# Kernel optimization log

Measured on AMD Instinct MI355X. Metric: run time of the kernel, lower is better.

Reference implementation:

```python
import jax, jax.numpy as jnp
import numpy as np

COST_POS = 5.0
COST_CONF = 1.0
LAMBDA_POS = 5.0
LAMBDA_CONF = 2.0
LAMBDA_NOOBJ = 0.5


def _lsa(cost):
    """Rectangular linear sum assignment (Jonker-Volgenant shortest augmenting
    path), same semantics as scipy.optimize.linear_sum_assignment."""
    cost = np.asarray(cost, dtype=np.float64)
    transposed = cost.shape[1] < cost.shape[0]
    if transposed:
        cost = cost.T
    nr, nc = cost.shape  # nr <= nc
    u = np.zeros(nr)
    v = np.zeros(nc)
    col4row = np.full(nr, -1, dtype=np.int64)
    row4col = np.full(nc, -1, dtype=np.int64)
    for cur_row in range(nr):
        shortest = np.full(nc, np.inf)
        pathback = np.full(nc, -1, dtype=np.int64)
        SR = np.zeros(nr, dtype=bool)
        SC = np.zeros(nc, dtype=bool)
        remaining = np.ones(nc, dtype=bool)
        min_val = 0.0
        i = cur_row
        sink = -1
        while sink == -1:
            SR[i] = True
            rem = np.flatnonzero(remaining)
            new_cost = min_val + cost[i, rem] - u[i] - v[rem]
            better = new_cost < shortest[rem]
            idx = rem[better]
            shortest[idx] = new_cost[better]
            pathback[idx] = i
            j = rem[np.argmin(shortest[rem])]
            min_val = shortest[j]
            remaining[j] = False
            SC[j] = True
            if row4col[j] == -1:
                sink = j
            else:
                i = row4col[j]
        u[cur_row] += min_val
        rows = np.flatnonzero(SR)
        rows = rows[rows != cur_row]
        u[rows] += min_val - shortest[col4row[rows]]
        v[SC] -= min_val - shortest[SC]
        j = sink
        while True:
            i = pathback[j]
            row4col[j] = i
            col4row[i], j = j, col4row[i]
            if i == cur_row:
                break
    if transposed:
        rows = col4row
        cols = np.arange(nr)
        order = np.argsort(rows)
        return rows[order], cols[order]
    return np.arange(nr), col4row


def _match(pred_c, conf, gt_c):
    """Per-image Hungarian matching (host-side, @no_grad in the original).
    cost = COST_POS * L1(pred, gt) - COST_CONF * sigmoid(conf)."""
    B, N, _ = pred_c.shape
    M = gt_c.shape[1]
    pred_idx = np.empty((B, M), dtype=np.int64)
    gt_idx = np.empty((B, M), dtype=np.int64)
    for b in range(B):
        c_pos = np.abs(pred_c[b][:, None, :] - gt_c[b][None, :, :]).sum(-1)  # [N,M]
        c_conf = -1.0 / (1.0 + np.exp(-conf[b]))  # [N]
        cost = COST_POS * c_pos + COST_CONF * c_conf[:, None]
        r, c = _lsa(cost)
        pred_idx[b] = r
        gt_idx[b] = c
    return pred_idx, gt_idx


def setup_inputs() -> dict:
    key = jax.random.key(0)
    B, N, M, D = 32, 300, 50, 2
    k1, k2, k3, k4, k5 = jax.random.split(key, 5)
    return {
        "pred_centroids": jax.random.uniform(k1, (B, N, D), dtype=jnp.float32),
        "pred_logits": jax.random.normal(k2, (B, N, 1), dtype=jnp.float32),
        "pred_conf": jax.random.normal(k3, (B, N), dtype=jnp.float32),
        "gt_centroids": jax.random.uniform(k4, (B, M, D), dtype=jnp.float32),
        "gt_classes": jax.random.randint(k5, (B, M), 0, 1),
    }


def reference(pred_centroids, pred_logits, pred_conf, gt_centroids, gt_classes):
    B, N, D = pred_centroids.shape
    M = gt_centroids.shape[1]
    # Matching indices are constants (computed under no_grad, host-side).
    pred_idx, gt_idx = _match(np.asarray(pred_centroids, np.float64),
                              np.asarray(pred_conf, np.float64),
                              np.asarray(gt_centroids, np.float64))
    pred_idx = jnp.asarray(pred_idx)  # [B,M]
    gt_idx = jnp.asarray(gt_idx)      # [B,M]
    b = jnp.arange(B)[:, None]
    mp = pred_centroids[b, pred_idx]  # [B,M,D]
    mg = gt_centroids[b, gt_idx]      # [B,M,D]
    # per-image L1 mean, summed over images (all images have M matches)
    loss_pos = jnp.mean(jnp.abs(mp - mg), axis=(1, 2)).sum()
    m_logit = pred_conf[b, pred_idx]  # [B,M]
    # BCE-with-logits, target=1: softplus(-x); target=0: softplus(x)
    loss_obj = jnp.mean(jax.nn.softplus(-m_logit), axis=1).sum()
    unmatched = jnp.ones((B, N), dtype=bool).at[b, pred_idx].set(False)
    sp = jax.nn.softplus(pred_conf)
    loss_noobj = (jnp.where(unmatched, sp, 0.0).sum(axis=1) / (N - M)).sum()
    loss_pos = LAMBDA_POS * loss_pos / B
    loss_conf_obj = LAMBDA_CONF * loss_obj / B
    loss_conf_noobj = LAMBDA_NOOBJ * loss_noobj / B
    loss_total = loss_pos + loss_conf_obj + loss_conf_noobj
    n_matched = jnp.asarray(float(M), dtype=jnp.float32)  # total matched / B
    return loss_pos, loss_conf_obj, loss_conf_noobj, loss_total, n_matched
```

## Files before the change

### kernel.cpp

```cpp
#include <hip/hip_runtime.h>
#include <math.h>


#define BB 32
#define NN 300
#define MM 50
#define KPL 5

#define F5(OP) OP(0) OP(1) OP(2) OP(3) OP(4)

__device__ __forceinline__ float softplus_f(float x) {
    return fmaxf(x, 0.0f) + __logf(1.0f + __expf(-fabsf(x)));
}
__device__ __forceinline__ float readlane_f(float x, int l) {
    return __int_as_float(__builtin_amdgcn_readlane(__float_as_int(x), l));
}
__device__ __forceinline__ int readlane_i(int x, int l) {
    return __builtin_amdgcn_readlane(x, l);
}
__device__ __forceinline__ unsigned umaxu(unsigned a, unsigned b) { return a > b ? a : b; }

__device__ __forceinline__ unsigned minkey_f32(float d) {
    unsigned s = (unsigned)__float_as_int(d);
    unsigned us = (s & 0x80000000u) ? ~s : (s | 0x80000000u);
    return ~us;
}
__device__ __forceinline__ float keydec_up(unsigned key) {
    unsigned us = (~key) | 0x1FFu;
    return (us & 0x80000000u) ? __uint_as_float(us & 0x7FFFFFFFu)
                              : __uint_as_float(~us);
}

__device__ __forceinline__ unsigned rowshr_maxkey(unsigned x) {
#define DPP_STEP(CTRL) { \
    unsigned t_ = (unsigned)__builtin_amdgcn_update_dpp(0, (int)x, CTRL, 0xF, 0xF, false); \
    x = umaxu(x, t_); }
    DPP_STEP(0x111)
    DPP_STEP(0x112)
    DPP_STEP(0x114)
    DPP_STEP(0x118)
#undef DPP_STEP
    return x;
}

__device__ __forceinline__ int div5(int n) { return (n * 52429) >> 18; }

__global__ __launch_bounds__(64, 1) void lsa_loss_kernel(
    const float* __restrict__ pred_c,
    const float* __restrict__ conf,
    const float* __restrict__ gt_c,
    float* __restrict__ ws)
{
    const int b = blockIdx.x;
    const int lane = threadIdx.x;
    const bool owns = lane < (NN / KPL);
    const int base_j = KPL * lane;

    __shared__ float4 s_px4[NN/4 + 1], s_py4[NN/4 + 1], s_cm4[NN/4 + 1];
    __shared__ int claimed[NN];
    float* s_px = (float*)s_px4;
    float* s_py = (float*)s_py4;
    float* s_cm2 = (float*)s_cm4;

#define DECL(k) float px5##k, py5##k, cf##k, cm##k, sh##k; int pb##k;
    F5(DECL)
#undef DECL
    unsigned r4cpack = 0;
    int rem;
    float u = 0.0f, gx5 = 0.0f, gy5 = 0.0f, u_sub = 0.0f;
    int col4row = -1;

#define LOADK(k) { \
        int j = base_j + k; \
        float vpx = 0.0f, vpy = 0.0f, vcf = 0.0f; \
        if (owns) { \
            float2 pc = *(const float2*)&pred_c[(b*NN + j)*2]; \
            vpx = pc.x; vpy = pc.y; \
            vcf = conf[b*NN + j]; \
        } \
        px5##k = 5.0f*vpx; py5##k = 5.0f*vpy; cf##k = vcf; \
        cm##k = -(1.0f / (1.0f + __expf(-vcf)));   }
    F5(LOADK)
#undef LOADK
    if (lane < MM) {
        float2 gc = *(const float2*)&gt_c[(b*MM + lane)*2];
        gx5 = 5.0f*gc.x;
        gy5 = 5.0f*gc.y;
    }
#define STAGE(k) if (owns) { int j = base_j + k; \
        s_px[j] = px5##k; s_py[j] = py5##k; s_cm2[j] = cm##k + 2.0f; \
        claimed[j] = 63; }
    F5(STAGE)
#undef STAGE
    if (lane == 63) {
        const float4 big = {1e30f, 1e30f, 1e30f, 1e30f};
        s_px4[NN/4] = big; s_py4[NN/4] = big; s_cm4[NN/4] = big;
    }
#define IDXF(k) const unsigned idx##k = (unsigned)(511 - (base_j + k));
    F5(IDXF)
#undef IDXF
    __syncthreads();

    unsigned bestkey = 0u;
#pragma unroll 2
    for (int j0 = 0; j0 < NN; j0 += 8) {
        float4 vxa = s_px4[(j0 >> 2) + 0], vxb = s_px4[(j0 >> 2) + 1];
        float4 vya = s_py4[(j0 >> 2) + 0], vyb = s_py4[(j0 >> 2) + 1];
        float4 vca = s_cm4[(j0 >> 2) + 0], vcb = s_cm4[(j0 >> 2) + 1];
        float c0 = fabsf(vxa.x - gx5) + fabsf(vya.x - gy5) + vca.x;
        float c1 = fabsf(vxa.y - gx5) + fabsf(vya.y - gy5) + vca.y;
        float c2 = fabsf(vxa.z - gx5) + fabsf(vya.z - gy5) + vca.z;
        float c3 = fabsf(vxa.w - gx5) + fabsf(vya.w - gy5) + vca.w;
        float c4 = fabsf(vxb.x - gx5) + fabsf(vyb.x - gy5) + vcb.x;
        float c5 = fabsf(vxb.y - gx5) + fabsf(vyb.y - gy5) + vcb.y;
        float c6 = fabsf(vxb.z - gx5) + fabsf(vyb.z - gy5) + vcb.z;
        float c7 = fabsf(vxb.w - gx5) + fabsf(vyb.w - gy5) + vcb.w;
        unsigned q0 = (~__float_as_uint(c0) & 0xFFFFFE00u) | (unsigned)(511 - j0);
        unsigned q1 = (~__float_as_uint(c1) & 0xFFFFFE00u) | (unsigned)(510 - j0);
        unsigned q2 = (~__float_as_uint(c2) & 0xFFFFFE00u) | (unsigned)(509 - j0);
        unsigned q3 = (~__float_as_uint(c3) & 0xFFFFFE00u) | (unsigned)(508 - j0);
        unsigned q4 = (~__float_as_uint(c4) & 0xFFFFFE00u) | (unsigned)(507 - j0);
        unsigned q5 = (~__float_as_uint(c5) & 0xFFFFFE00u) | (unsigned)(506 - j0);
        unsigned q6 = (~__float_as_uint(c6) & 0xFFFFFE00u) | (unsigned)(505 - j0);
        unsigned q7 = (~__float_as_uint(c7) & 0xFFFFFE00u) | (unsigned)(504 - j0);
        unsigned qa = umaxu(umaxu(q0, q1), umaxu(q2, q3));
        unsigned qb = umaxu(umaxu(q4, q5), umaxu(q6, q7));
        bestkey = umaxu(bestkey, umaxu(qa, qb));
    }
    int wantj = 511 - (int)(bestkey & 511u);
    if (lane < MM) {
        u = fabsf(s_px[wantj] - gx5) + fabsf(s_py[wantj] - gy5)
            + (s_cm2[wantj] - 2.0f);
        atomicMin(&claimed[wantj], lane);
    }
    __syncthreads();
    if (lane < MM && claimed[wantj] == lane) col4row = wantj;
#define RCINIT(k) { int w = owns ? claimed[base_j + k] : 63; \
        r4cpack |= ((w < 63) ? (unsigned)(w + 1) : 0u) << (6*k); }
    F5(RCINIT)
#undef RCINIT

    unsigned long long freerows = __ballot(lane < MM && col4row < 0);
    while (freerows) {
        int cur_row = (int)__ffsll(freerows) - 1;
        freerows &= freerows - 1ull;

#define RINIT(k) sh##k = INFINITY; pb##k = 0;
        F5(RINIT)
#undef RINIT
        rem = owns ? 0x1F : 0;
        unsigned long long sr_mask = 0ull;
        float min_val = 0.0f;
        int i = cur_row;
        int sink = -1;

        for (int pops = 0; pops <= NN && sink < 0; ++pops) {
            sr_mask |= (1ull << i);
            float u_i   = readlane_f(u,   i);
            float gx5_i = readlane_f(gx5, i);
            float gy5_i = readlane_f(gy5, i);
            float mvu = min_val - u_i;
            int ip1 = i + 1;

#define RELAX(k) { \
                float dx5 = fabsf(px5##k - gx5_i); \
                float dy5 = fabsf(py5##k - gy5_i); \
                float nc = dx5 + dy5 + (cm##k + mvu); \
                bool imp = (((rem >> k) & 1) != 0) && (nc < sh##k); \
                sh##k = imp ? nc : sh##k; \
                pb##k = imp ? ip1 : pb##k; }
            F5(RELAX)
#undef RELAX

#define KEYK(k) unsigned key##k = ((rem >> k) & 1) \
                ? ((minkey_f32(sh##k) & 0xFFFFFE00u) | idx##k) : 0u;
            F5(KEYK)
#undef KEYK
            unsigned lkey = umaxu(umaxu(umaxu(key0, key1), umaxu(key2, key3)), key4);

            unsigned acc = rowshr_maxkey(lkey);
            unsigned k0 = (unsigned)readlane_i((int)acc, 15);
            unsigned k1 = (unsigned)readlane_i((int)acc, 31);
            unsigned k2 = (unsigned)readlane_i((int)acc, 47);
            unsigned k3 = (unsigned)readlane_i((int)acc, 63);
            unsigned gkey = umaxu(umaxu(k0, k1), umaxu(k2, k3));
            if (gkey == 0u) { sink = 0; break; }

            int bestj = 511 - (int)(gkey & 511u);
            int srcl = div5(bestj);
            int qj = bestj - KPL*srcl;
            min_val = keydec_up(gkey);

            unsigned rp = (unsigned)readlane_i((int)r4cpack, srcl);
            int r4 = (int)((rp >> (qj*6)) & 63u) - 1;

            rem = (lane == srcl) ? (rem & ~(1 << qj)) : rem;
            if (r4 < 0 || r4 >= MM) {
                sink = bestj;
            } else {
                i = r4;
                u_sub = (lane == r4) ? min_val : u_sub;
            }
        }

        if (lane < MM) {
            if (lane == cur_row) u += min_val;
            else if ((sr_mask >> lane) & 1ull) u += min_val - u_sub;
        }
#define VUPD(k) if (owns && !((rem >> k) & 1)) cm##k += min_val - sh##k;
        F5(VUPD)
#undef VUPD

        int j = sink < 0 ? 0 : sink;
        for (int step = 0; step <= MM; ++step) {
            int tj = div5(j), qj2 = j - KPL*tj;
            int pbl = qj2==0?pb0:qj2==1?pb1:qj2==2?pb2:qj2==3?pb3:pb4;
            int pi = readlane_i(pbl, tj) - 1;
            if (pi < 0 || pi >= MM) break;
            int q6 = qj2*6;
            unsigned nv = (r4cpack & ~(63u << q6)) | ((unsigned)(pi+1) << q6);
            r4cpack = (lane == tj) ? nv : r4cpack;
            int c_old = readlane_i(col4row, pi);
            col4row = (lane == pi) ? j : col4row;
            j = c_old;
            if (pi == cur_row) break;
            if (j < 0 || j >= NN) break;
        }
    }

    float lp = 0.0f, lo = 0.0f, ln = 0.0f;
    if (lane < MM) {
        int j = (col4row < 0 || col4row >= NN) ? 0 : col4row;
        lp = 0.2f * (fabsf(s_px[j] - gx5) + fabsf(s_py[j] - gy5));
        lo = softplus_f(-conf[b*NN + j]);
    }
#define NOOBJ(k) if (owns && ((r4cpack >> (6*k)) & 63u) == 0u) \
        ln += softplus_f(cf##k);
    F5(NOOBJ)
#undef NOOBJ
    for (int off = 32; off > 0; off >>= 1) {
        lp += __shfl_xor(lp, off, 64);
        lo += __shfl_xor(lo, off, 64);
        ln += __shfl_xor(ln, off, 64);
    }
    if (lane == 0) {
        ws[b*4 + 0] = lp;
        ws[b*4 + 1] = lo;
        ws[b*4 + 2] = ln;
    }
}

__global__ __launch_bounds__(64, 1) void reduce_out_kernel(
    const float* __restrict__ ws, float* __restrict__ out)
{
    const int lane = threadIdx.x;
    float lp = 0.0f, lo = 0.0f, ln = 0.0f;
    if (lane < BB) {
        lp = ws[lane*4 + 0];
        lo = ws[lane*4 + 1];
        ln = ws[lane*4 + 2];
    }
    for (int off = 16; off > 0; off >>= 1) {
        lp += __shfl_xor(lp, off, 64);
        lo += __shfl_xor(lo, off, 64);
        ln += __shfl_xor(ln, off, 64);
    }
    if (lane == 0) {
        double cp = 5.0 * ((double)lp / (double)(MM*2))  / (double)BB;
        double co = 2.0 * ((double)lo / (double)MM)      / (double)BB;
        double cn = 0.5 * ((double)ln / (double)(NN-MM)) / (double)BB;
        out[0] = (float)cp;
        out[1] = (float)co;
        out[2] = (float)cn;
        out[3] = (float)(cp + co + cn);
        out[4] = 50.0f;
    }
}

extern "C" void kernel_launch(void* const* d_in, const int* in_sizes, int n_in,
                              void* d_out, int out_size, void* d_ws, size_t ws_size,
                              hipStream_t stream) {
    const float* pred_c = (const float*)d_in[0];
    const float* conf   = (const float*)d_in[2];
    const float* gt_c   = (const float*)d_in[3];
    float* out = (float*)d_out;
    float* ws  = (float*)d_ws;

    lsa_loss_kernel<<<BB, 64, 0, stream>>>(pred_c, conf, gt_c, ws);
    reduce_out_kernel<<<1, 64, 0, stream>>>(ws, out);
}
```

Baseline: 92.95 us.

## Split greedy initial column scan across four wavefronts per block

Launches 256 threads per image so four wavefronts each scan an 80-column slice of the cost matrix for the initial row-minimum pass, then merges the partial best keys through shared memory before wave 0 continues the augmenting-path phase alone. The shared padding is extended so the last slice reads sentinel values. Confidence logits are also staged in shared memory, so the final objectness loss reads from LDS instead of global memory. This adds a block barrier and idle waves during the serial Hungarian phase. The speedup is limited to the init scan, which is a small part of the total.

```diff
diff --git a/kernel.cpp b/kernel.cpp
--- a/kernel.cpp
+++ b/kernel.cpp
@@ -6,6 +6,8 @@
 #define NN 300
 #define MM 50
 #define KPL 5
+#define NWV 4
+#define CPW 80
 
 #define F5(OP) OP(0) OP(1) OP(2) OP(3) OP(4)
 
@@ -45,19 +47,23 @@
 
 __device__ __forceinline__ int div5(int n) { return (n * 52429) >> 18; }
 
-__global__ __launch_bounds__(64, 1) void lsa_loss_kernel(
+__global__ __launch_bounds__(NWV*64, 1) void lsa_loss_kernel(
     const float* __restrict__ pred_c,
     const float* __restrict__ conf,
     const float* __restrict__ gt_c,
     float* __restrict__ ws)
 {
     const int b = blockIdx.x;
-    const int lane = threadIdx.x;
-    const bool owns = lane < (NN / KPL);
-    const int base_j = KPL * lane;
-
-    __shared__ float4 s_px4[NN/4 + 1], s_py4[NN/4 + 1], s_cm4[NN/4 + 1];
+    const int tid = threadIdx.x;
+    const int wid = tid >> 6;
+    const int lane = tid & 63;
+    const bool owns = tid < (NN / KPL);
+    const int base_j = KPL * tid;
+
+    __shared__ float4 s_px4[NN/4 + 5], s_py4[NN/4 + 5], s_cm4[NN/4 + 5];
     __shared__ int claimed[NN];
+    __shared__ float s_cf[NN];
+    __shared__ unsigned s_part[NWV * 64];
     float* s_px = (float*)s_px4;
     float* s_py = (float*)s_py4;
     float* s_cm2 = (float*)s_cm4;
@@ -89,12 +95,13 @@
     }
 #define STAGE(k) if (owns) { int j = base_j + k; \
         s_px[j] = px5##k; s_py[j] = py5##k; s_cm2[j] = cm##k + 2.0f; \
-        claimed[j] = 63; }
+        s_cf[j] = cf##k; claimed[j] = 63; }
     F5(STAGE)
 #undef STAGE
-    if (lane == 63) {
+    if (tid >= 59 && tid < 64) {
         const float4 big = {1e30f, 1e30f, 1e30f, 1e30f};
-        s_px4[NN/4] = big; s_py4[NN/4] = big; s_cm4[NN/4] = big;
+        int p = 75 + (tid - 59);
+        s_px4[p] = big; s_py4[p] = big; s_cm4[p] = big;
     }
 #define IDXF(k) const unsigned idx##k = (unsigned)(511 - (base_j + k));
     F5(IDXF)
@@ -102,8 +109,9 @@
     __syncthreads();
 
     unsigned bestkey = 0u;
-#pragma unroll 2
-    for (int j0 = 0; j0 < NN; j0 += 8) {
+#pragma unroll
+    for (int t = 0; t < CPW/8; ++t) {
+        int j0 = wid*CPW + t*8;
         float4 vxa = s_px4[(j0 >> 2) + 0], vxb = s_px4[(j0 >> 2) + 1];
         float4 vya = s_py4[(j0 >> 2) + 0], vyb = s_py4[(j0 >> 2) + 1];
         float4 vca = s_cm4[(j0 >> 2) + 0], vcb = s_cm4[(j0 >> 2) + 1];
@@ -127,14 +135,26 @@
         unsigned qb = umaxu(umaxu(q4, q5), umaxu(q6, q7));
         bestkey = umaxu(bestkey, umaxu(qa, qb));
     }
-    int wantj = 511 - (int)(bestkey & 511u);
-    if (lane < MM) {
-        u = fabsf(s_px[wantj] - gx5) + fabsf(s_py[wantj] - gy5)
-            + (s_cm2[wantj] - 2.0f);
-        atomicMin(&claimed[wantj], lane);
-    }
+    s_part[wid*64 + lane] = bestkey;
     __syncthreads();
-    if (lane < MM && claimed[wantj] == lane) col4row = wantj;
+
+    if (wid == 0) {
+        bestkey = umaxu(umaxu(s_part[lane], s_part[64 + lane]),
+                        umaxu(s_part[128 + lane], s_part[192 + lane]));
+        int wantj = 511 - (int)(bestkey & 511u);
+        if (lane < MM) {
+            u = fabsf(s_px[wantj] - gx5) + fabsf(s_py[wantj] - gy5)
+                + (s_cm2[wantj] - 2.0f);
+            atomicMin(&claimed[wantj], lane);
+        }
+        col4row = -1 - wantj;
+    }
+    __syncthreads();
+    if (wid != 0) return;
+    {
+        int wantj = -1 - col4row;
+        col4row = (lane < MM && claimed[wantj] == lane) ? wantj : -1;
+    }
 #define RCINIT(k) { int w = owns ? claimed[base_j + k] : 63; \
         r4cpack |= ((w < 63) ? (unsigned)(w + 1) : 0u) << (6*k); }
     F5(RCINIT)
@@ -232,7 +252,7 @@
     if (lane < MM) {
         int j = (col4row < 0 || col4row >= NN) ? 0 : col4row;
         lp = 0.2f * (fabsf(s_px[j] - gx5) + fabsf(s_py[j] - gy5));
-        lo = softplus_f(-conf[b*NN + j]);
+        lo = softplus_f(-s_cf[j]);
     }
 #define NOOBJ(k) if (owns && ((r4cpack >> (6*k)) & 63u) == 0u) \
         ln += softplus_f(cf##k);
@@ -286,6 +306,6 @@
     float* out = (float*)d_out;
     float* ws  = (float*)d_ws;
 
-    lsa_loss_kernel<<<BB, 64, 0, stream>>>(pred_c, conf, gt_c, ws);
+    lsa_loss_kernel<<<BB, NWV*64, 0, stream>>>(pred_c, conf, gt_c, ws);
     reduce_out_kernel<<<1, 64, 0, stream>>>(ws, out);
 }
```

After: 86.95 us. 6.5% less time.
